# Performance work log

Hardware: AMD Instinct MI355X
Metric: run time of the kernel (lower is better)

The kernel has to match this reference:

```python
import jax, jax.numpy as jnp
import numpy as np

B, C = 4096, 16384
SCALE = 16.0
MARGIN = 0.1
NEG_INF = -10000.0
HARD_SCALE = 1.0 + 0.012
HARD_SHIFT = 0.012


def setup_inputs() -> dict:
    key = jax.random.key(0)
    k1, k2, k3 = jax.random.split(key, 3)
    inputs = jax.random.normal(k1, (B, C), dtype=jnp.float32)
    targets = jax.random.randint(k2, (B,), 0, C, dtype=jnp.int64)
    # camera-positive mask: 0/1 floats
    pos_cam_mask = jax.random.bernoulli(k3, 0.5, (B, C)).astype(jnp.float32)
    mask = jnp.zeros((B, C), dtype=bool)  # unused by the module (overwritten)
    return {"inputs": inputs, "targets": targets, "mask": mask, "pos_cam_mask": pos_cam_mask}


def reference(inputs, targets, mask, pos_cam_mask):
    b, c = inputs.shape
    rows = jnp.arange(b)
    one_hot = jax.nn.one_hot(targets, c, dtype=inputs.dtype)  # (B, C)
    # camera-masked logits; non-positive-cam entries pushed to -10000
    cam_inputs = pos_cam_mask * inputs + (1.0 - pos_cam_mask) * NEG_INF
    gt = inputs[rows, targets]  # (B,) target logit, pre-modification
    hard_mask = cam_inputs >= gt[:, None]  # (B, C)
    # rescale hard examples: x <- 1.012 * x + 0.012 where hard
    x = jnp.where(hard_mask, HARD_SCALE * inputs + HARD_SHIFT, inputs)
    # restore original gt logit at target positions (scatter_)
    x = jnp.where(one_hot > 0, gt[:, None], x)
    output = SCALE * (x - one_hot * MARGIN)
    # mean cross-entropy
    logp = jax.nn.log_softmax(output, axis=-1)
    loss = -jnp.mean(logp[rows, targets])
    return loss
```

## Files before the change

kernel.cpp:

```cpp
#include <hip/hip_runtime.h>


#define B_ 4096
#define C_ 16384
#define LOG2E 1.44269504088896340736f

__global__ __launch_bounds__(256, 3) void coscam_loss_kernel(
    const float* __restrict__ inputs,
    const int*   __restrict__ targets,
    const float* __restrict__ pos_mask,
    float*       __restrict__ out)
{
    const int row = blockIdx.x;
    const int tid = threadIdx.x;

    const float* __restrict__ rin = inputs   + (size_t)row * C_;
    const float* __restrict__ rpm = pos_mask + (size_t)row * C_;

    const int   t     = targets[row];
    const float gt    = rin[t];
    const float pos_t = rpm[t];

    const float wt      = gt - 0.1f;
    const float out_t   = 16.0f * wt;
    const float shift   = fmaxf(out_t, 40.0f);
    const float nshift2 = -shift * LOG2E;
    const float k16l2e  = 16.0f * LOG2E;

    float4 xs[16], ps[16];
    #pragma unroll
    for (int u = 0; u < 16; ++u) {
        const int c = u * 1024 + tid * 4;
        xs[u] = *(const float4*)(rin + c);
        ps[u] = *(const float4*)(rpm + c);
    }

    float acc0 = 0.0f, acc1 = 0.0f, acc2 = 0.0f, acc3 = 0.0f;
    #pragma unroll
    for (int u = 0; u < 16; ++u) {
        const float4 x4 = xs[u];
        const float4 p4 = ps[u];
        const float w0 = ((p4.x > 0.5f) && (x4.x >= gt)) ? fmaf(1.012f, x4.x, 0.012f) : x4.x;
        const float w1 = ((p4.y > 0.5f) && (x4.y >= gt)) ? fmaf(1.012f, x4.y, 0.012f) : x4.y;
        const float w2 = ((p4.z > 0.5f) && (x4.z >= gt)) ? fmaf(1.012f, x4.z, 0.012f) : x4.z;
        const float w3 = ((p4.w > 0.5f) && (x4.w >= gt)) ? fmaf(1.012f, x4.w, 0.012f) : x4.w;
        acc0 += __builtin_amdgcn_exp2f(fmaf(w0, k16l2e, nshift2));
        acc1 += __builtin_amdgcn_exp2f(fmaf(w1, k16l2e, nshift2));
        acc2 += __builtin_amdgcn_exp2f(fmaf(w2, k16l2e, nshift2));
        acc3 += __builtin_amdgcn_exp2f(fmaf(w3, k16l2e, nshift2));
    }

    float s = (acc0 + acc1) + (acc2 + acc3);

    #pragma unroll
    for (int off = 32; off > 0; off >>= 1)
        s += __shfl_down(s, off);

    __shared__ float red_s[4];
    const int wave = tid >> 6;
    const int lane = tid & 63;
    if (lane == 0) red_s[wave] = s;
    __syncthreads();

    if (tid == 0) {
        float total = (red_s[0] + red_s[1]) + (red_s[2] + red_s[3]);
        const float w_wrong = (pos_t > 0.5f) ? fmaf(1.012f, gt, 0.012f) : gt;
        total += __builtin_amdgcn_exp2f(fmaf(wt,      k16l2e, nshift2))
               - __builtin_amdgcn_exp2f(fmaf(w_wrong, k16l2e, nshift2));
        const float loss_row = (__logf(total) + shift) - out_t;
        atomicAdd(out, loss_row * (1.0f / (float)B_));
    }
}

extern "C" void kernel_launch(void* const* d_in, const int* in_sizes, int n_in,
                              void* d_out, int out_size, void* d_ws, size_t ws_size,
                              hipStream_t stream) {
    const float* inputs   = (const float*)d_in[0];
    const int*   targets  = (const int*)  d_in[1];
    const float* pos_mask = (const float*)d_in[3];
    float* out = (float*)d_out;

    (void)hipMemsetAsync(out, 0, sizeof(float), stream);

    coscam_loss_kernel<<<dim3(B_), dim3(256), 0, stream>>>(inputs, targets, pos_mask, out);
}
```

Baseline: 597.4 us.

## Stream row tiles through per-wave LDS ring via async global-to-LDS loads

Instead of loading all 16 float4 tiles of inputs and mask into registers up front, each wave owns a contiguous quarter of the row. It streams 256-element chunks into a four-deep LDS ring using global_load_lds, with explicit vmcnt waits between consuming and refilling slots. The goal is to cut the large register footprint, raise occupancy and overlap loads with the exp2 work. In exchange each wave keeps fewer loads in flight, uses 32 KB of LDS per block, and relies on hand-written waitcnt values. A ring slot is refilled right after it is read, with no LDS ordering barrier between the read and the new write.

```diff
diff --git a/kernel.cpp b/kernel.cpp
--- a/kernel.cpp
+++ b/kernel.cpp
@@ -1,18 +1,29 @@
 #include <hip/hip_runtime.h>
+#include <stdint.h>
 
 
 #define B_ 4096
 #define C_ 16384
 #define LOG2E 1.44269504088896340736f
 
-__global__ __launch_bounds__(256, 3) void coscam_loss_kernel(
+#define WAIT_VM(n) __builtin_amdgcn_s_waitcnt((n) | (7u << 4) | (15u << 8))
+
+typedef __attribute__((address_space(1))) const void gas_void;
+typedef __attribute__((address_space(3))) void las_void;
+
+__global__ __launch_bounds__(256) void coscam_loss_kernel(
     const float* __restrict__ inputs,
     const int*   __restrict__ targets,
     const float* __restrict__ pos_mask,
     float*       __restrict__ out)
 {
-    const int row = blockIdx.x;
-    const int tid = threadIdx.x;
+    const int row  = blockIdx.x;
+    const int tid  = threadIdx.x;
+    const int wave = tid >> 6;
+    const int lane = tid & 63;
+
+    __shared__ float stage[4][2][4][256];
+    __shared__ float red_s[4];
 
     const float* __restrict__ rin = inputs   + (size_t)row * C_;
     const float* __restrict__ rpm = pos_mask + (size_t)row * C_;
@@ -27,19 +38,22 @@
     const float nshift2 = -shift * LOG2E;
     const float k16l2e  = 16.0f * LOG2E;
 
-    float4 xs[16], ps[16];
-    #pragma unroll
-    for (int u = 0; u < 16; ++u) {
-        const int c = u * 1024 + tid * 4;
-        xs[u] = *(const float4*)(rin + c);
-        ps[u] = *(const float4*)(rpm + c);
-    }
+    const float* wx = rin + wave * 4096;
+    const float* wp = rpm + wave * 4096;
+    const int    lo = lane * 4;
 
     float acc0 = 0.0f, acc1 = 0.0f, acc2 = 0.0f, acc3 = 0.0f;
-    #pragma unroll
-    for (int u = 0; u < 16; ++u) {
-        const float4 x4 = xs[u];
-        const float4 p4 = ps[u];
+
+    auto issue = [&](int k) {
+        __builtin_amdgcn_global_load_lds((gas_void*)(wx + (k << 8) + lo),
+                                         (las_void*)&stage[wave][0][k & 3][0], 16, 0, 0);
+        __builtin_amdgcn_global_load_lds((gas_void*)(wp + (k << 8) + lo),
+                                         (las_void*)&stage[wave][1][k & 3][0], 16, 0, 0);
+    };
+
+    auto consume = [&](int k) {
+        const float4 x4 = *(const float4*)&stage[wave][0][k & 3][lo];
+        const float4 p4 = *(const float4*)&stage[wave][1][k & 3][lo];
         const float w0 = ((p4.x > 0.5f) && (x4.x >= gt)) ? fmaf(1.012f, x4.x, 0.012f) : x4.x;
         const float w1 = ((p4.y > 0.5f) && (x4.y >= gt)) ? fmaf(1.012f, x4.y, 0.012f) : x4.y;
         const float w2 = ((p4.z > 0.5f) && (x4.z >= gt)) ? fmaf(1.012f, x4.z, 0.012f) : x4.z;
@@ -48,7 +62,20 @@
         acc1 += __builtin_amdgcn_exp2f(fmaf(w1, k16l2e, nshift2));
         acc2 += __builtin_amdgcn_exp2f(fmaf(w2, k16l2e, nshift2));
         acc3 += __builtin_amdgcn_exp2f(fmaf(w3, k16l2e, nshift2));
+    };
+
+    issue(0); issue(1); issue(2); issue(3);
+
+    #pragma unroll
+    for (int k = 0; k < 12; ++k) {
+        WAIT_VM(6);
+        consume(k);
+        issue(k + 4);
     }
+    WAIT_VM(6); consume(12);
+    WAIT_VM(4); consume(13);
+    WAIT_VM(2); consume(14);
+    WAIT_VM(0); consume(15);
 
     float s = (acc0 + acc1) + (acc2 + acc3);
 
@@ -56,9 +83,6 @@
     for (int off = 32; off > 0; off >>= 1)
         s += __shfl_down(s, off);
 
-    __shared__ float red_s[4];
-    const int wave = tid >> 6;
-    const int lane = tid & 63;
     if (lane == 0) red_s[wave] = s;
     __syncthreads();
 
```

Measured after the change: 601.6 us. No clear change (+0.7%).
